# Kernel tuning notes

Measured on AMD Instinct MI355X. Metric: run time of the kernel, lower is better.

Reference implementation:

```python
import jax, jax.numpy as jnp
import numpy as np

TEMPERATURE = 0.1
EPS = 1e-8  # matches torch F.cosine_similarity norm clamp

N, D = 4096, 256

def setup_inputs() -> dict:
    key = jax.random.key(0)
    k1, k2 = jax.random.split(key)
    z_i = jax.random.normal(k1, (N, D), dtype=jnp.float32)
    z_j = jax.random.normal(k2, (N, D), dtype=jnp.float32)
    return {"z_i": z_i, "z_j": z_j}

def reference(z_i, z_j):
    n = z_i.shape[0]
    z = jnp.concatenate([z_i, z_j], axis=0)              # [2N, D]
    # cosine similarity via normalized Gram matrix (faithful to F.cosine_similarity)
    norms = jnp.maximum(jnp.linalg.norm(z, axis=-1, keepdims=True), EPS)
    zn = z / norms                                        # [2N, D]
    sim = (zn @ zn.T) / TEMPERATURE                       # [2N, 2N]
    # mask self-similarity on the diagonal
    diag = jnp.eye(2 * n, dtype=bool)
    sim = jnp.where(diag, -jnp.inf, sim)
    # labels: positive of i is i+N (and vice versa)
    labels = jnp.concatenate([jnp.arange(n, 2 * n), jnp.arange(0, n)])
    logp = jax.nn.log_softmax(sim, axis=-1)               # [2N, 2N]
    nll = -jnp.take_along_axis(logp, labels[:, None], axis=-1)[:, 0]
    return jnp.mean(nll)
```

## Files before the change

kernel.cpp:

```cpp
#include <hip/hip_runtime.h>
#include <hip/hip_bf16.h>

#define NHALF 4096
#define TWO_N 8192
#define DDIM 256
#define INV_T 10.0f
#define SCALE 14.426950408889634f
#define KBSTRIDE ((size_t)TWO_N * 64)

typedef __bf16 v8bf __attribute__((ext_vector_type(8)));
typedef float f32x4 __attribute__((ext_vector_type(4)));

#if __has_builtin(__builtin_amdgcn_exp2f)
#define EXP2F(x) __builtin_amdgcn_exp2f(x)
#else
#define EXP2F(x) exp2f(x)
#endif

static __device__ __forceinline__ unsigned int f2bf(float x) {
    __hip_bfloat16 h = __float2bfloat16(x);
    return (unsigned int)*(unsigned short*)&h;
}

__global__ __launch_bounds__(256) void ntx_norm_kernel(
    const float* __restrict__ zi, const float* __restrict__ zj,
    char* __restrict__ znB, float* __restrict__ rowacc,
    float* __restrict__ out) {
    const int w = threadIdx.x >> 6;
    const int lane = threadIdx.x & 63;
    const int r = blockIdx.x * 4 + w;
    const float* src = (r < NHALF) ? (zi + (size_t)r * DDIM)
                                   : (zj + (size_t)(r - NHALF) * DDIM);
    float4 v = ((const float4*)src)[lane];
    float ss = v.x * v.x + v.y * v.y + v.z * v.z + v.w * v.w;
#pragma unroll
    for (int m = 1; m < 64; m <<= 1) ss += __shfl_xor(ss, m);
    float rinv = 1.0f / fmaxf(sqrtf(ss), 1e-8f);
    uint2 pk;
    pk.x = f2bf(v.x * rinv) | (f2bf(v.y * rinv) << 16);
    pk.y = f2bf(v.z * rinv) | (f2bf(v.w * rinv) << 16);
    char* dst = znB + (size_t)(lane >> 3) * KBSTRIDE + (size_t)r * 64 +
                ((lane >> 1) & 3) * 16 + (lane & 1) * 8;
    *(uint2*)dst = pk;
    if (blockIdx.x < 32) rowacc[blockIdx.x * 256 + threadIdx.x] = 0.0f;
    if (blockIdx.x == 0 && threadIdx.x == 0) out[0] = 0.0f;
}

__global__ __launch_bounds__(64, 2) void ntx_gram_kernel(
    const char* __restrict__ znB,
    float* __restrict__ rowacc,
    float* __restrict__ spos) {
    const int lane = threadIdx.x;
    const int lrow = lane & 15, lk = lane >> 4;

    bool odg[4];
#pragma unroll
    for (int j = 0; j < 4; ++j) odg[j] = (lrow == lk * 4 + j);

    f32x4 af[4][8], bf[8], acc[4];
    float rowsum[4][4];
    int rbase;

#define LOAD_AF()                                                             \
    do {                                                                      \
        _Pragma("unroll")                                                     \
        for (int rf = 0; rf < 4; ++rf) {                                      \
            const char* ab =                                                  \
                znB + (size_t)(rbase + rf * 16 + lrow) * 64 + lk * 16;        \
            _Pragma("unroll")                                                 \
            for (int kb = 0; kb < 8; ++kb)                                    \
                af[rf][kb] = *(const f32x4*)(ab + kb * KBSTRIDE);             \
        }                                                                     \
        _Pragma("unroll")                                                     \
        for (int rf = 0; rf < 4; ++rf)                                        \
            _Pragma("unroll")                                                 \
            for (int kb = 0; kb < 8; ++kb)                                    \
                asm volatile("" : "+v"(af[rf][kb]));                 \
    } while (0)

#define ZERO_RS()                                                             \
    do {                                                                      \
        _Pragma("unroll")                                                     \
        for (int rf = 0; rf < 4; ++rf)                                        \
            _Pragma("unroll")                                                 \
            for (int j = 0; j < 4; ++j) rowsum[rf][j] = 0.0f;                 \
    } while (0)

#define LOADB(cf)                                                             \
    do {                                                                      \
        _Pragma("unroll")                                                     \
        for (int kb = 0; kb < 8; ++kb)                                        \
            bf[kb] = *(const f32x4*)(zcb + (cf) * 1024 + kb * KBSTRIDE);      \
    } while (0)

#define MFMAB()                                                               \
    do {                                                                      \
        _Pragma("unroll")                                                     \
        for (int rf = 0; rf < 4; ++rf) acc[rf] = (f32x4){0.f, 0.f, 0.f, 0.f}; \
        __builtin_amdgcn_s_setprio(1);                                        \
        _Pragma("unroll")                                                     \
        for (int kb = 0; kb < 8; ++kb) {                                      \
            _Pragma("unroll")                                                 \
            for (int rf = 0; rf < 4; ++rf)                                    \
                acc[rf] = __builtin_amdgcn_mfma_f32_16x16x32_bf16(            \
                    __builtin_bit_cast(v8bf, af[rf][kb]),                     \
                    __builtin_bit_cast(v8bf, bf[kb]), acc[rf], 0, 0, 0);      \
        }                                                                     \
        __builtin_amdgcn_s_setprio(0);                                        \
    } while (0)

#define EPI(cf, SELF, POSB, cbase)                                            \
    do {                                                                      \
        float fce[4];                                                         \
        _Pragma("unroll")                                                     \
        for (int rf = 0; rf < 4; ++rf) {                                      \
            const bool dfrag = (rf == (cf));                                  \
            float p = 0.0f;                                                   \
            _Pragma("unroll")                                                 \
            for (int j = 0; j < 4; ++j) {                                     \
                const float sv = acc[rf][j];                                  \
                const bool od = dfrag && odg[j];                              \
                if ((POSB) && od) {                                           \
                    const int u = rf * 16 + lk * 4 + j;                       \
                    spos[rbase + u] = sv * INV_T;                             \
                    spos[(cbase) + u] = sv * INV_T;                           \
                }                                                             \
                float e = EXP2F(sv * SCALE);                                  \
                e = ((SELF) && od) ? 0.0f : e;                                \
                rowsum[rf][j] += e;                                           \
                p += e;                                                       \
            }                                                                 \
            fce[rf] = p;                                                      \
        }                                                                     \
        if (!(SELF)) {                                                        \
            float ce = (fce[0] + fce[1]) + (fce[2] + fce[3]);                 \
            ce += __shfl_xor(ce, 16);                                         \
            ce += __shfl_xor(ce, 32);                                         \
            if (lane < 16)                                                    \
                atomicAdd(&rowacc[(cbase) + (cf) * 16 + lrow], ce);           \
        }                                                                     \
    } while (0)

#define DO_TILE(dd, SELF, POSB)                                               \
    do {                                                                      \
        const int ct = (((rbase >> 6) - (dd)) + 128) & 127;                   \
        const int cb = ct * 64;                                               \
        const char* zcb = znB + (size_t)(cb + lrow) * 64 + lk * 16;           \
        LOADB(0);                                                             \
        MFMAB(); LOADB(1); EPI(0, SELF, POSB, cb);                            \
        MFMAB(); LOADB(2); EPI(1, SELF, POSB, cb);                            \
        MFMAB(); LOADB(3); EPI(2, SELF, POSB, cb);                            \
        MFMAB();           EPI(3, SELF, POSB, cb);                            \
    } while (0)

#define FLUSH_RS()                                                            \
    do {                                                                      \
        _Pragma("unroll")                                                     \
        for (int rf = 0; rf < 4; ++rf) {                                      \
            _Pragma("unroll")                                                 \
            for (int j = 0; j < 4; ++j) {                                     \
                float v = rowsum[rf][j];                                      \
                v += __shfl_xor(v, 1);                                        \
                v += __shfl_xor(v, 2);                                        \
                v += __shfl_xor(v, 4);                                        \
                v += __shfl_xor(v, 8);                                        \
                if (lrow == 0)                                                \
                    atomicAdd(&rowacc[rbase + rf * 16 + lk * 4 + j], v);      \
            }                                                                 \
        }                                                                     \
    } while (0)

    if (blockIdx.x < 16) {
#pragma unroll 1
        for (int s = 0; s < 4; ++s) {
            rbase = (blockIdx.x * 4 + s) * 64;
            LOAD_AF();
            ZERO_RS();
            DO_TILE(64, false, true);
            FLUSH_RS();
        }
    } else {
        const int t = blockIdx.x - 16;
        const int rt = t >> 4, g = t & 15;
        rbase = rt * 64;
        LOAD_AF();
        ZERO_RS();
#pragma unroll 1
        for (int s = 0; s < 4; ++s) {
            const int d = g * 4 + s;
            const bool self = (d == 0);
            DO_TILE(d, self, false);
        }
        FLUSH_RS();
    }
#undef LOAD_AF
#undef ZERO_RS
#undef LOADB
#undef MFMAB
#undef EPI
#undef DO_TILE
#undef FLUSH_RS
}

__global__ __launch_bounds__(256) void ntx_final_kernel(
    const float* __restrict__ rowacc, const float* __restrict__ spos,
    float* __restrict__ out) {
    const int tid = threadIdx.x;
    const int r = blockIdx.x * 256 + tid;
    float nll = logf(rowacc[r]) - spos[r];
    __shared__ float red[256];
    red[tid] = nll;
    __syncthreads();
    for (int s = 128; s > 0; s >>= 1) {
        if (tid < s) red[tid] += red[tid + s];
        __syncthreads();
    }
    if (tid == 0) atomicAdd(out, red[0] * (1.0f / (float)TWO_N));
}

extern "C" void kernel_launch(void* const* d_in, const int* in_sizes, int n_in,
                              void* d_out, int out_size, void* d_ws, size_t ws_size,
                              hipStream_t stream) {
    const float* zi = (const float*)d_in[0];
    const float* zj = (const float*)d_in[1];
    char* ws = (char*)d_ws;
    char* znB = ws;
    size_t off = (size_t)TWO_N * DDIM * 2;
    float* spos = (float*)(ws + off);
    off += (size_t)TWO_N * 4;
    float* rowacc = (float*)(ws + off);
    float* out = (float*)d_out;

    ntx_norm_kernel<<<TWO_N / 4, 256, 0, stream>>>(zi, zj, znB, rowacc, out);
    ntx_gram_kernel<<<2064, 64, 0, stream>>>(znB, rowacc, spos);
    ntx_final_kernel<<<TWO_N / 256, 256, 0, stream>>>(rowacc, spos, out);
}
```

Baseline: 50.81 us.

## Pack four wave tasks per block and double-buffer B fragments across tiles

The Gram kernel now runs four independent wave-level tasks per 256-thread block instead of one task per 64-thread block. B-fragment loads are double-buffered (bfA/bfB) two column fragments ahead, and the 16 column fragments of the four diagonal tiles are fully unrolled into one continuous pipeline. This hides global-load latency behind MFMA and epilogue work and removes per-tile loop overhead. The cost is an extra 8 VGPR vectors per wave, higher register pressure that may reduce occupancy under launch_bounds(256,2), and a larger code size.

```diff
diff --git a/kernel.cpp b/kernel.cpp
--- a/kernel.cpp
+++ b/kernel.cpp
@@ -46,27 +46,28 @@
     if (blockIdx.x == 0 && threadIdx.x == 0) out[0] = 0.0f;
 }
 
-__global__ __launch_bounds__(64, 2) void ntx_gram_kernel(
+__global__ __launch_bounds__(256, 2) void ntx_gram_kernel(
     const char* __restrict__ znB,
     float* __restrict__ rowacc,
     float* __restrict__ spos) {
-    const int lane = threadIdx.x;
+    const int tid = threadIdx.x;
+    const int w = tid >> 6, lane = tid & 63;
+    const int task = blockIdx.x * 4 + w;
     const int lrow = lane & 15, lk = lane >> 4;
 
     bool odg[4];
 #pragma unroll
     for (int j = 0; j < 4; ++j) odg[j] = (lrow == lk * 4 + j);
 
-    f32x4 af[4][8], bf[8], acc[4];
+    f32x4 af[4][8], bfA[8], bfB[8], acc[4];
     float rowsum[4][4];
-    int rbase;
-
-#define LOAD_AF()                                                             \
+
+#define LOAD_AF(RB)                                                           \
     do {                                                                      \
         _Pragma("unroll")                                                     \
         for (int rf = 0; rf < 4; ++rf) {                                      \
             const char* ab =                                                  \
-                znB + (size_t)(rbase + rf * 16 + lrow) * 64 + lk * 16;        \
+                znB + (size_t)((RB) + rf * 16 + lrow) * 64 + lk * 16;         \
             _Pragma("unroll")                                                 \
             for (int kb = 0; kb < 8; ++kb)                                    \
                 af[rf][kb] = *(const f32x4*)(ab + kb * KBSTRIDE);             \
@@ -86,14 +87,14 @@
             for (int j = 0; j < 4; ++j) rowsum[rf][j] = 0.0f;                 \
     } while (0)
 
-#define LOADB(cf)                                                             \
+#define LOADB(BUF, ZP, cf)                                                    \
     do {                                                                      \
         _Pragma("unroll")                                                     \
         for (int kb = 0; kb < 8; ++kb)                                        \
-            bf[kb] = *(const f32x4*)(zcb + (cf) * 1024 + kb * KBSTRIDE);      \
-    } while (0)
-
-#define MFMAB()                                                               \
+            BUF[kb] = *(const f32x4*)((ZP) + (cf) * 1024 + kb * KBSTRIDE);    \
+    } while (0)
+
+#define MFMAB(BUF)                                                            \
     do {                                                                      \
         _Pragma("unroll")                                                     \
         for (int rf = 0; rf < 4; ++rf) acc[rf] = (f32x4){0.f, 0.f, 0.f, 0.f}; \
@@ -104,12 +105,12 @@
             for (int rf = 0; rf < 4; ++rf)                                    \
                 acc[rf] = __builtin_amdgcn_mfma_f32_16x16x32_bf16(            \
                     __builtin_bit_cast(v8bf, af[rf][kb]),                     \
-                    __builtin_bit_cast(v8bf, bf[kb]), acc[rf], 0, 0, 0);      \
+                    __builtin_bit_cast(v8bf, BUF[kb]), acc[rf], 0, 0, 0);     \
         }                                                                     \
         __builtin_amdgcn_s_setprio(0);                                        \
     } while (0)
 
-#define EPI(cf, SELF, POSB, cbase)                                            \
+#define EPI(cf, CB, SELF, POSB, RB)                                           \
     do {                                                                      \
         float fce[4];                                                         \
         _Pragma("unroll")                                                     \
@@ -122,8 +123,8 @@
                 const bool od = dfrag && odg[j];                              \
                 if ((POSB) && od) {                                           \
                     const int u = rf * 16 + lk * 4 + j;                       \
-                    spos[rbase + u] = sv * INV_T;                             \
-                    spos[(cbase) + u] = sv * INV_T;                           \
+                    spos[(RB) + u] = sv * INV_T;                              \
+                    spos[(CB) + u] = sv * INV_T;                              \
                 }                                                             \
                 float e = EXP2F(sv * SCALE);                                  \
                 e = ((SELF) && od) ? 0.0f : e;                                \
@@ -137,23 +138,11 @@
             ce += __shfl_xor(ce, 16);                                         \
             ce += __shfl_xor(ce, 32);                                         \
             if (lane < 16)                                                    \
-                atomicAdd(&rowacc[(cbase) + (cf) * 16 + lrow], ce);           \
-        }                                                                     \
-    } while (0)
-
-#define DO_TILE(dd, SELF, POSB)                                               \
-    do {                                                                      \
-        const int ct = (((rbase >> 6) - (dd)) + 128) & 127;                   \
-        const int cb = ct * 64;                                               \
-        const char* zcb = znB + (size_t)(cb + lrow) * 64 + lk * 16;           \
-        LOADB(0);                                                             \
-        MFMAB(); LOADB(1); EPI(0, SELF, POSB, cb);                            \
-        MFMAB(); LOADB(2); EPI(1, SELF, POSB, cb);                            \
-        MFMAB(); LOADB(3); EPI(2, SELF, POSB, cb);                            \
-        MFMAB();           EPI(3, SELF, POSB, cb);                            \
-    } while (0)
-
-#define FLUSH_RS()                                                            \
+                atomicAdd(&rowacc[(CB) + (cf) * 16 + lrow], ce);              \
+        }                                                                     \
+    } while (0)
+
+#define FLUSH_RS(RB)                                                          \
     do {                                                                      \
         _Pragma("unroll")                                                     \
         for (int rf = 0; rf < 4; ++rf) {                                      \
@@ -165,40 +154,66 @@
                 v += __shfl_xor(v, 4);                                        \
                 v += __shfl_xor(v, 8);                                        \
                 if (lrow == 0)                                                \
-                    atomicAdd(&rowacc[rbase + rf * 16 + lk * 4 + j], v);      \
+                    atomicAdd(&rowacc[(RB) + rf * 16 + lk * 4 + j], v);       \
             }                                                                 \
         }                                                                     \
     } while (0)
 
-    if (blockIdx.x < 16) {
+    if (task < 16) {
 #pragma unroll 1
         for (int s = 0; s < 4; ++s) {
-            rbase = (blockIdx.x * 4 + s) * 64;
-            LOAD_AF();
+            const int rb = (task * 4 + s) * 64;
+            const int cb = rb + 4096;
+            LOAD_AF(rb);
             ZERO_RS();
-            DO_TILE(64, false, true);
-            FLUSH_RS();
+            const char* zp = znB + (size_t)(cb + lrow) * 64 + lk * 16;
+            LOADB(bfA, zp, 0);
+            LOADB(bfB, zp, 1);
+            MFMAB(bfA); LOADB(bfA, zp, 2); EPI(0, cb, false, true, rb);
+            MFMAB(bfB); LOADB(bfB, zp, 3); EPI(1, cb, false, true, rb);
+            MFMAB(bfA);                    EPI(2, cb, false, true, rb);
+            MFMAB(bfB);                    EPI(3, cb, false, true, rb);
+            FLUSH_RS(rb);
         }
     } else {
-        const int t = blockIdx.x - 16;
+        const int t = task - 16;
         const int rt = t >> 4, g = t & 15;
-        rbase = rt * 64;
-        LOAD_AF();
+        const int rbase = rt * 64;
+        LOAD_AF(rbase);
         ZERO_RS();
-#pragma unroll 1
+        const char* zps[4];
+        int cbs[4];
+#pragma unroll
         for (int s = 0; s < 4; ++s) {
             const int d = g * 4 + s;
-            const bool self = (d == 0);
-            DO_TILE(d, self, false);
+            const int ct = ((rt - d) + 128) & 127;
+            cbs[s] = ct * 64;
+            zps[s] = znB + (size_t)(cbs[s] + lrow) * 64 + lk * 16;
         }
-        FLUSH_RS();
+        const bool g0 = (g == 0);
+
+        LOADB(bfA, zps[0], 0);
+        LOADB(bfB, zps[0], 1);
+#define RSTEP(st, CUR)                                                        \
+    do {                                                                      \
+        MFMAB(CUR);                                                           \
+        if ((st) + 2 < 16)                                                    \
+            LOADB(CUR, zps[((st) + 2) >> 2], ((st) + 2) & 3);                 \
+        EPI(((st) & 3), cbs[(st) >> 2], (g0 && ((st) >> 2) == 0), false,      \
+            rbase);                                                           \
+    } while (0)
+        RSTEP(0, bfA);  RSTEP(1, bfB);  RSTEP(2, bfA);  RSTEP(3, bfB);
+        RSTEP(4, bfA);  RSTEP(5, bfB);  RSTEP(6, bfA);  RSTEP(7, bfB);
+        RSTEP(8, bfA);  RSTEP(9, bfB);  RSTEP(10, bfA); RSTEP(11, bfB);
+        RSTEP(12, bfA); RSTEP(13, bfB); RSTEP(14, bfA); RSTEP(15, bfB);
+#undef RSTEP
+        FLUSH_RS(rbase);
     }
 #undef LOAD_AF
 #undef ZERO_RS
 #undef LOADB
 #undef MFMAB
 #undef EPI
-#undef DO_TILE
 #undef FLUSH_RS
 }
 
@@ -232,6 +247,6 @@
     float* out = (float*)d_out;
 
     ntx_norm_kernel<<<TWO_N / 4, 256, 0, stream>>>(zi, zj, znB, rowacc, out);
-    ntx_gram_kernel<<<2064, 64, 0, stream>>>(znB, rowacc, spos);
+    ntx_gram_kernel<<<516, 256, 0, stream>>>(znB, rowacc, spos);
     ntx_final_kernel<<<TWO_N / 256, 256, 0, stream>>>(rowacc, spos, out);
 }
```

Measured after the change: 131.0 us. 2.58x slower.

## Pack four gram tasks per block and double-buffer B fragment loads

Applied to the files above, without the earlier changes.

The gram kernel now runs four independent wave-level tasks per 256-thread block instead of one task per 64-thread block, cutting the grid from 2064 to 516 blocks. B fragments are double-buffered (two register sets) so the next fragment's loads are issued before the current MFMA and epilogue, deepening load prefetch. The setprio hints are dropped, and the per-fragment column sum is accumulated directly. Register pressure rises with two B buffers under launch_bounds(256,2), which may cause spills or lower occupancy.

```diff
diff --git a/kernel.cpp b/kernel.cpp
--- a/kernel.cpp
+++ b/kernel.cpp
@@ -46,18 +46,20 @@
     if (blockIdx.x == 0 && threadIdx.x == 0) out[0] = 0.0f;
 }
 
-__global__ __launch_bounds__(64, 2) void ntx_gram_kernel(
+__global__ __launch_bounds__(256, 2) void ntx_gram_kernel(
     const char* __restrict__ znB,
     float* __restrict__ rowacc,
     float* __restrict__ spos) {
-    const int lane = threadIdx.x;
+    const int tid = threadIdx.x;
+    const int w = tid >> 6, lane = tid & 63;
+    const int task = blockIdx.x * 4 + w;
     const int lrow = lane & 15, lk = lane >> 4;
 
     bool odg[4];
 #pragma unroll
     for (int j = 0; j < 4; ++j) odg[j] = (lrow == lk * 4 + j);
 
-    f32x4 af[4][8], bf[8], acc[4];
+    f32x4 af[4][8];
     float rowsum[4][4];
     int rbase;
 
@@ -75,7 +77,7 @@
         for (int rf = 0; rf < 4; ++rf)                                        \
             _Pragma("unroll")                                                 \
             for (int kb = 0; kb < 8; ++kb)                                    \
-                asm volatile("" : "+v"(af[rf][kb]));                 \
+                asm volatile("" : "+v"(af[rf][kb]));  \
     } while (0)
 
 #define ZERO_RS()                                                             \
@@ -86,18 +88,18 @@
             for (int j = 0; j < 4; ++j) rowsum[rf][j] = 0.0f;                 \
     } while (0)
 
-#define LOADB(cf)                                                             \
+#define LOADB(bf, cf)                                                         \
     do {                                                                      \
         _Pragma("unroll")                                                     \
         for (int kb = 0; kb < 8; ++kb)                                        \
             bf[kb] = *(const f32x4*)(zcb + (cf) * 1024 + kb * KBSTRIDE);      \
     } while (0)
 
-#define MFMAB()                                                               \
-    do {                                                                      \
+#define COMPUTE_EPI(bf, cf)                                                   \
+    do {                                                                      \
+        f32x4 acc[4];                                                         \
         _Pragma("unroll")                                                     \
         for (int rf = 0; rf < 4; ++rf) acc[rf] = (f32x4){0.f, 0.f, 0.f, 0.f}; \
-        __builtin_amdgcn_s_setprio(1);                                        \
         _Pragma("unroll")                                                     \
         for (int kb = 0; kb < 8; ++kb) {                                      \
             _Pragma("unroll")                                                 \
@@ -106,38 +108,30 @@
                     __builtin_bit_cast(v8bf, af[rf][kb]),                     \
                     __builtin_bit_cast(v8bf, bf[kb]), acc[rf], 0, 0, 0);      \
         }                                                                     \
-        __builtin_amdgcn_s_setprio(0);                                        \
-    } while (0)
-
-#define EPI(cf, SELF, POSB, cbase)                                            \
-    do {                                                                      \
-        float fce[4];                                                         \
+        float ce = 0.0f;                                                      \
         _Pragma("unroll")                                                     \
         for (int rf = 0; rf < 4; ++rf) {                                      \
             const bool dfrag = (rf == (cf));                                  \
-            float p = 0.0f;                                                   \
             _Pragma("unroll")                                                 \
             for (int j = 0; j < 4; ++j) {                                     \
                 const float sv = acc[rf][j];                                  \
                 const bool od = dfrag && odg[j];                              \
-                if ((POSB) && od) {                                           \
+                if (posb && od) {                                             \
                     const int u = rf * 16 + lk * 4 + j;                       \
                     spos[rbase + u] = sv * INV_T;                             \
-                    spos[(cbase) + u] = sv * INV_T;                           \
+                    spos[cb + u] = sv * INV_T;                                \
                 }                                                             \
                 float e = EXP2F(sv * SCALE);                                  \
-                e = ((SELF) && od) ? 0.0f : e;                                \
+                e = (self && od) ? 0.0f : e;                                  \
                 rowsum[rf][j] += e;                                           \
-                p += e;                                                       \
+                ce += e;                                                      \
             }                                                                 \
-            fce[rf] = p;                                                      \
-        }                                                                     \
-        if (!(SELF)) {                                                        \
-            float ce = (fce[0] + fce[1]) + (fce[2] + fce[3]);                 \
+        }                                                                     \
+        if (!self) {                                                          \
             ce += __shfl_xor(ce, 16);                                         \
             ce += __shfl_xor(ce, 32);                                         \
             if (lane < 16)                                                    \
-                atomicAdd(&rowacc[(cbase) + (cf) * 16 + lrow], ce);           \
+                atomicAdd(&rowacc[cb + (cf) * 16 + lrow], ce);                \
         }                                                                     \
     } while (0)
 
@@ -145,12 +139,18 @@
     do {                                                                      \
         const int ct = (((rbase >> 6) - (dd)) + 128) & 127;                   \
         const int cb = ct * 64;                                               \
+        const bool self = (SELF);                                             \
+        const bool posb = (POSB);                                             \
         const char* zcb = znB + (size_t)(cb + lrow) * 64 + lk * 16;           \
-        LOADB(0);                                                             \
-        MFMAB(); LOADB(1); EPI(0, SELF, POSB, cb);                            \
-        MFMAB(); LOADB(2); EPI(1, SELF, POSB, cb);                            \
-        MFMAB(); LOADB(3); EPI(2, SELF, POSB, cb);                            \
-        MFMAB();           EPI(3, SELF, POSB, cb);                            \
+        f32x4 bfA[8], bfB[8];                                                 \
+        LOADB(bfA, 0);                                                        \
+        LOADB(bfB, 1);                                                        \
+        COMPUTE_EPI(bfA, 0);                                                  \
+        LOADB(bfA, 2);                                                        \
+        COMPUTE_EPI(bfB, 1);                                                  \
+        LOADB(bfB, 3);                                                        \
+        COMPUTE_EPI(bfA, 2);                                                  \
+        COMPUTE_EPI(bfB, 3);                                                  \
     } while (0)
 
 #define FLUSH_RS()                                                            \
@@ -170,17 +170,17 @@
         }                                                                     \
     } while (0)
 
-    if (blockIdx.x < 16) {
+    if (task < 16) {
 #pragma unroll 1
         for (int s = 0; s < 4; ++s) {
-            rbase = (blockIdx.x * 4 + s) * 64;
+            rbase = (task * 4 + s) * 64;
             LOAD_AF();
             ZERO_RS();
             DO_TILE(64, false, true);
             FLUSH_RS();
         }
     } else {
-        const int t = blockIdx.x - 16;
+        const int t = task - 16;
         const int rt = t >> 4, g = t & 15;
         rbase = rt * 64;
         LOAD_AF();
@@ -188,16 +188,14 @@
 #pragma unroll 1
         for (int s = 0; s < 4; ++s) {
             const int d = g * 4 + s;
-            const bool self = (d == 0);
-            DO_TILE(d, self, false);
+            DO_TILE(d, d == 0, false);
         }
         FLUSH_RS();
     }
 #undef LOAD_AF
 #undef ZERO_RS
 #undef LOADB
-#undef MFMAB
-#undef EPI
+#undef COMPUTE_EPI
 #undef DO_TILE
 #undef FLUSH_RS
 }
@@ -232,6 +230,6 @@
     float* out = (float*)d_out;
 
     ntx_norm_kernel<<<TWO_N / 4, 256, 0, stream>>>(zi, zj, znB, rowacc, out);
-    ntx_gram_kernel<<<2064, 64, 0, stream>>>(znB, rowacc, spos);
+    ntx_gram_kernel<<<516, 256, 0, stream>>>(znB, rowacc, spos);
     ntx_final_kernel<<<TWO_N / 256, 256, 0, stream>>>(rowacc, spos, out);
 }
```

Result: slower. 54.49 us (median of 2 runs) (+7.3%).
